# Kernel tuning notes

Hardware: AMD Instinct MI355X
Metric: run time of the kernel (lower is better)

The kernel has to match this reference:

```python
import jax, jax.numpy as jnp
import numpy as np
from jax import lax

DN = ('NCDHW', 'OIDHW', 'NCDHW')
BN_EPS = 1e-5
COS_EPS = 1e-8   # torch CosineSimilarity eps
L1_EPS = 1e-12   # F.normalize default eps


def _lrelu(x):
    return jnp.where(x >= 0, x, 0.2 * x)


def _bn(x, g, b):
    # BatchNorm3d in training mode: batch statistics over (N, D, H, W)
    m = jnp.mean(x, axis=(0, 2, 3, 4), keepdims=True)
    v = jnp.var(x, axis=(0, 2, 3, 4), keepdims=True)
    return g[None, :, None, None, None] * (x - m) * lax.rsqrt(v + BN_EPS) + b[None, :, None, None, None]


def _conv(x, w, b, stride):
    y = lax.conv_general_dilated(x, w, window_strides=stride, padding=[(1, 1)] * 3,
                                 dimension_numbers=DN)
    return y + b[None, :, None, None, None]


def _convT(x, w, b, stride, out_pad):
    # ConvTranspose3d(k=3, padding=1, output_padding=out_pad) == input-dilated conv
    # with flipped kernel and padding (k-1-p, k-1-p+op) = (1, 1+op).
    k = jnp.flip(w, axis=(2, 3, 4))
    y = lax.conv_general_dilated(x, k, window_strides=(1, 1, 1),
                                 padding=[(1, 1 + o) for o in out_pad],
                                 lhs_dilation=stride, dimension_numbers=DN)
    return y + b[None, :, None, None, None]


def setup_inputs() -> dict:
    key = jax.random.key(0)
    ks = jax.random.split(key, 20)
    d = {}
    d['x'] = jax.random.normal(ks[0], (2, 1, 16, 256, 256), jnp.float32)
    enc = [(96, 1), (128, 96), (256, 128), (256, 256)]
    for i, (co, ci) in enumerate(enc):
        fan = ci * 27
        d[f'enc_w{i+1}'] = jax.random.normal(ks[1 + i], (co, ci, 3, 3, 3), jnp.float32) * np.float32(np.sqrt(2.0 / fan))
        d[f'enc_b{i+1}'] = jnp.zeros((co,), jnp.float32)
        d[f'enc_g{i+1}'] = jnp.ones((co,), jnp.float32)
        d[f'enc_be{i+1}'] = jnp.zeros((co,), jnp.float32)
    d['mem'] = jax.random.normal(ks[5], (2000, 256), jnp.float32) * np.float32(1.0 / np.sqrt(256))
    dec = [(256, 256), (128, 256), (96, 128), (1, 96)]  # (Cout, Cin)
    for i, (co, ci) in enumerate(dec):
        fan = ci * 27
        d[f'dec_w{i+1}'] = jax.random.normal(ks[6 + i], (co, ci, 3, 3, 3), jnp.float32) * np.float32(np.sqrt(2.0 / fan))
        d[f'dec_b{i+1}'] = jnp.zeros((co,), jnp.float32)
        if i < 3:
            d[f'dec_g{i+1}'] = jnp.ones((co,), jnp.float32)
            d[f'dec_be{i+1}'] = jnp.zeros((co,), jnp.float32)
    return d


def _forward(x,
             enc_w1, enc_b1, enc_g1, enc_be1,
             enc_w2, enc_b2, enc_g2, enc_be2,
             enc_w3, enc_b3, enc_g3, enc_be3,
             enc_w4, enc_b4, enc_g4, enc_be4,
             mem,
             dec_w1, dec_b1, dec_g1, dec_be1,
             dec_w2, dec_b2, dec_g2, dec_be2,
             dec_w3, dec_b3, dec_g3, dec_be3,
             dec_w4, dec_b4):
    # ---- encoder ----
    f = _lrelu(_bn(_conv(x, enc_w1, enc_b1, (1, 2, 2)), enc_g1, enc_be1))
    f = _lrelu(_bn(_conv(f, enc_w2, enc_b2, (2, 2, 2)), enc_g2, enc_be2))
    f = _lrelu(_bn(_conv(f, enc_w3, enc_b3, (2, 2, 2)), enc_g3, enc_be3))
    f = _lrelu(_bn(_conv(f, enc_w4, enc_b4, (2, 2, 2)), enc_g4, enc_be4))
    # ---- memory addressing (cosine similarity without materializing repeats) ----
    N, C, D, H, W = f.shape
    z = f.transpose(0, 2, 3, 4, 1).reshape(-1, C)                    # [M, C]
    z_norm = jnp.linalg.norm(z, axis=1, keepdims=True)               # [M, 1]
    m_norm = jnp.linalg.norm(mem, axis=1, keepdims=True)             # [K, 1]
    num = z @ mem.T                                                  # [M, K]
    den = jnp.maximum(z_norm * m_norm.T, COS_EPS)
    w = jax.nn.softmax(num / den, axis=1)
    w_hat = jax.nn.relu(w)
    w_hat = w_hat / jnp.maximum(jnp.sum(jnp.abs(w_hat), axis=1, keepdims=True), L1_EPS)
    z_hat = w_hat @ mem                                              # [M, C]
    zf = z_hat.reshape(N, D, H, W, C).transpose(0, 4, 1, 2, 3)
    # ---- decoder ----
    y = _lrelu(_bn(_convT(zf, dec_w1, dec_b1, (2, 2, 2), (1, 1, 1)), dec_g1, dec_be1))
    y = _lrelu(_bn(_convT(y, dec_w2, dec_b2, (2, 2, 2), (1, 1, 1)), dec_g2, dec_be2))
    y = _lrelu(_bn(_convT(y, dec_w3, dec_b3, (2, 2, 2), (1, 1, 1)), dec_g3, dec_be3))
    out = _convT(y, dec_w4, dec_b4, (1, 2, 2), (0, 1, 1))
    return out, w_hat


def reference(x,
              enc_w1, enc_b1, enc_g1, enc_be1,
              enc_w2, enc_b2, enc_g2, enc_be2,
              enc_w3, enc_b3, enc_g3, enc_be3,
              enc_w4, enc_b4, enc_g4, enc_be4,
              mem,
              dec_w1, dec_b1, dec_g1, dec_be1,
              dec_w2, dec_b2, dec_g2, dec_be2,
              dec_w3, dec_b3, dec_g3, dec_be3,
              dec_w4, dec_b4):
    return _forward(x,
                    enc_w1, enc_b1, enc_g1, enc_be1,
                    enc_w2, enc_b2, enc_g2, enc_be2,
                    enc_w3, enc_b3, enc_g3, enc_be3,
                    enc_w4, enc_b4, enc_g4, enc_be4,
                    mem,
                    dec_w1, dec_b1, dec_g1, dec_be1,
                    dec_w2, dec_b2, dec_g2, dec_be2,
                    dec_w3, dec_b3, dec_g3, dec_be3,
                    dec_w4, dec_b4)
```

## Files before the change

kernel.cpp:

```cpp
#include <hip/hip_runtime.h>
#include <math.h>

typedef unsigned short u16;
typedef __bf16 bf16;
typedef bf16 bf16x8 __attribute__((ext_vector_type(8)));
typedef float f32x4 __attribute__((ext_vector_type(4)));
typedef u16 u16x8 __attribute__((ext_vector_type(8)));

__device__ inline float b2f(u16 u){ unsigned x = ((unsigned)u) << 16; return __builtin_bit_cast(float, x); }
__device__ inline u16 f2b(float f){ bf16 b = (bf16)f; return __builtin_bit_cast(u16, b); }
__device__ inline f32x4 mfma16(bf16x8 a, bf16x8 b, f32x4 c){
    return __builtin_amdgcn_mfma_f32_16x16x32_bf16(a, b, c, 0, 0, 0);
}
__device__ inline void unp8(uint4 v, float* f){
    f[0]=__builtin_bit_cast(float, v.x<<16); f[1]=__builtin_bit_cast(float, v.x&0xffff0000u);
    f[2]=__builtin_bit_cast(float, v.y<<16); f[3]=__builtin_bit_cast(float, v.y&0xffff0000u);
    f[4]=__builtin_bit_cast(float, v.z<<16); f[5]=__builtin_bit_cast(float, v.z&0xffff0000u);
    f[6]=__builtin_bit_cast(float, v.w<<16); f[7]=__builtin_bit_cast(float, v.w&0xffff0000u);
}

struct Rep7 {
    const float* src[7];
    u16* dst[7];
    int co[7];
    int ci[7];
};
__global__ __launch_bounds__(256) void repack7_k(Rep7 a)
{
    int w = blockIdx.y;
    const float* src = a.src[w]; u16* dst = a.dst[w];
    int Co = a.co[w], Ci = a.ci[w];
    int tot = 27 * Co * Ci;
    for (int e = blockIdx.x * 256 + threadIdx.x; e < tot; e += gridDim.x * 256) {
        int ci = e % Ci; int t2 = e / Ci; int co = t2 % Co; int tp = t2 / Co;
        dst[e] = f2b(src[(size_t)(co * Ci + ci) * 27 + tp]);
    }
}

template<bool ISCONV, int CK, int BN>
__global__ __launch_bounds__(512) void conv_mfma3_k(
    const u16* __restrict__ in, const u16* __restrict__ wt,
    const float* __restrict__ bias, u16* __restrict__ out,
    float* __restrict__ pm, float* __restrict__ pv,
    int Ci, int Co, int Di, int Hi, int Wi,
    int ld, int lh, int lw, int Do, int Ho, int Wo)
{
    constexpr int NK = CK / 32;
    constexpr int NF = BN / 32;
    __shared__ u16 As[128][CK + 8];
    __shared__ u16 Bs[BN][CK + 8];
    const int tid = threadIdx.x;
    const int mtile = blockIdx.x, co0 = blockIdx.y * BN;
    int pd = 0, ph = 0, pw = 0;
    if (!ISCONV) { int bz = blockIdx.z; pd = bz >> 2; ph = (bz >> 1) & 1; pw = bz & 1; }

    const int arow = tid >> 2, seg = tid & 3;
    int xo, yo, zo, n;
    { int m = mtile * 128 + arow;
      xo = m & ((1 << lw) - 1); m >>= lw;
      yo = m & ((1 << lh) - 1); m >>= lh;
      zo = m & ((1 << ld) - 1); n = m >> ld; }
    const bool isb = arow < BN;

    const int wave = tid >> 6, lane = tid & 63;
    const int wm = wave >> 1, wn = wave & 1;
    const int fr = lane & 15, fs = lane >> 4;

    f32x4 acc[2][NF];
    #pragma unroll
    for (int mf = 0; mf < 2; ++mf)
        #pragma unroll
        for (int nf = 0; nf < NF; ++nf) acc[mf][nf] = f32x4{0,0,0,0};

    const int ntd = ISCONV ? 3 : pd + 1;
    const int nth = ISCONV ? 3 : ph + 1;
    const int ntw = ISCONV ? 3 : pw + 1;
    const int nck = Ci / CK;
    const int T = ntd * nth * ntw * nck;
    const size_t HiWi = (size_t)Hi * Wi;

    int pjd = 0, pjh = 0, pjw = 0, pck = 0;
    uint4 av[NK], bv[NK];

    auto load_panel = [&]() {
        int zi = ISCONV ? 2 * zo + pjd - 1 : zo + (pd ? pjd : 0);
        int wd = ISCONV ? pjd : (pd ? (pjd ? 0 : 2) : 1);
        int yi = ISCONV ? 2 * yo + pjh - 1 : yo + (ph ? pjh : 0);
        int wh = ISCONV ? pjh : (ph ? (pjh ? 0 : 2) : 1);
        int xi = ISCONV ? 2 * xo + pjw - 1 : xo + (pw ? pjw : 0);
        int ww = ISCONV ? pjw : (pw ? (pjw ? 0 : 2) : 1);
        bool va = ((unsigned)zi < (unsigned)Di) && ((unsigned)yi < (unsigned)Hi) &&
                  ((unsigned)xi < (unsigned)Wi);
        size_t abase = 0;
        if (va) abase = (((size_t)(n * Di + zi)) * HiWi + (size_t)yi * Wi + xi) * Ci
                      + (size_t)pck * CK;
        int widx = wd * 9 + wh * 3 + ww;
        size_t bbase = ((size_t)widx * Co + (co0 + arow)) * (size_t)Ci + (size_t)pck * CK;
        #pragma unroll
        for (int k = 0; k < NK; ++k) {
            int col = k * 32 + seg * 8;
            av[k] = va  ? *reinterpret_cast<const uint4*>(in + abase + col) : uint4{0,0,0,0};
            bv[k] = isb ? *reinterpret_cast<const uint4*>(wt + bbase + col) : uint4{0,0,0,0};
        }
        ++pck;
        if (pck == nck) { pck = 0; ++pjw;
            if (pjw == ntw) { pjw = 0; ++pjh;
                if (pjh == nth) { pjh = 0; ++pjd; } } }
    };

    load_panel();
    for (int it = 0; it < T; ++it) {
        __syncthreads();
        #pragma unroll
        for (int k = 0; k < NK; ++k) {
            *reinterpret_cast<uint4*>(&As[arow][k * 32 + seg * 8]) = av[k];
            if (isb) *reinterpret_cast<uint4*>(&Bs[arow][k * 32 + seg * 8]) = bv[k];
        }
        __syncthreads();
        if (it + 1 < T) load_panel();
        #pragma unroll
        for (int k = 0; k < NK; ++k) {
            bf16x8 a0 = *reinterpret_cast<const bf16x8*>(&As[wm * 32      + fr][k * 32 + fs * 8]);
            bf16x8 a1 = *reinterpret_cast<const bf16x8*>(&As[wm * 32 + 16 + fr][k * 32 + fs * 8]);
            #pragma unroll
            for (int nf = 0; nf < NF; ++nf) {
                bf16x8 b = *reinterpret_cast<const bf16x8*>(
                    &Bs[wn * (BN / 2) + nf * 16 + fr][k * 32 + fs * 8]);
                acc[0][nf] = mfma16(a0, b, acc[0][nf]);
                acc[1][nf] = mfma16(a1, b, acc[1][nf]);
            }
        }
    }

    float bi[NF], s[NF], q[NF];
    #pragma unroll
    for (int nf = 0; nf < NF; ++nf) {
        bi[nf] = bias[co0 + wn * (BN / 2) + nf * 16 + fr];
        s[nf] = 0.f; q[nf] = 0.f;
    }
    #pragma unroll
    for (int mf = 0; mf < 2; ++mf) {
        #pragma unroll
        for (int j = 0; j < 4; ++j) {
            int rm = mtile * 128 + wm * 32 + mf * 16 + fs * 4 + j;
            size_t vox;
            if (ISCONV) vox = (size_t)rm;
            else {
                int X = rm & ((1 << lw) - 1); int m2 = rm >> lw;
                int Y = m2 & ((1 << lh) - 1); m2 >>= lh;
                int Z = m2 & ((1 << ld) - 1); int nn = m2 >> ld;
                vox = (((size_t)(nn * Do + (2 * Z + pd))) * Ho + (2 * Y + ph)) * Wo + (2 * X + pw);
            }
            #pragma unroll
            for (int nf = 0; nf < NF; ++nf) {
                float f = acc[mf][nf][j] + bi[nf];
                out[vox * Co + (co0 + wn * (BN / 2) + nf * 16 + fr)] = f2b(f);
                s[nf] += f; q[nf] += f * f;
            }
        }
    }
    __syncthreads();
    float* bnS = reinterpret_cast<float*>(&As[0][0]);
    float* bnQ = bnS + BN * 16;
    #pragma unroll
    for (int nf = 0; nf < NF; ++nf) {
        int cl = wn * (BN / 2) + nf * 16 + fr;
        bnS[cl * 16 + wm * 4 + fs] = s[nf];
        bnQ[cl * 16 + wm * 4 + fs] = q[nf];
    }
    __syncthreads();
    if (tid < BN) {
        float S = 0.f, Q = 0.f;
        #pragma unroll
        for (int i = 0; i < 16; ++i) { S += bnS[tid * 16 + i]; Q += bnQ[tid * 16 + i]; }
        int p = blockIdx.x + gridDim.x * (blockIdx.y + gridDim.y * blockIdx.z);
        pm[(size_t)p * BN + tid] = S;
        pv[(size_t)p * BN + tid] = Q;
    }
}

__global__ __launch_bounds__(256) void enc1_k(
    const float* __restrict__ x, const float* __restrict__ w,
    const float* __restrict__ bias, u16* __restrict__ out)
{
    __shared__ uint4 smem[256 * 13];
    float* Xi = reinterpret_cast<float*>(smem);
    const int tid = threadIdx.x;
    int t = blockIdx.x;
    const int tx = t & 7; t >>= 3;
    const int ty = t & 15; t >>= 4;
    const int tz = t;
    const int n = blockIdx.y;
    const int z0 = tz * 2, y0 = ty * 8, x0 = tx * 16;
    for (int i = tid; i < 2244; i += 256) {
        int fz = i / 561; int r = i - fz * 561; int fy = r / 33; int fx = r - fy * 33;
        int zi = z0 - 1 + fz, yi = 2 * y0 - 1 + fy, xi = 2 * x0 - 1 + fx;
        float v = 0.f;
        if ((unsigned)zi < 16u && (unsigned)yi < 256u && (unsigned)xi < 256u)
            v = x[((size_t)(n * 16 + zi) * 256 + yi) * 256 + xi];
        Xi[i] = v;
    }
    __syncthreads();
    const int lx = tid & 15, ly = (tid >> 4) & 7, lz = tid >> 7;
    float iv[27];
    #pragma unroll
    for (int kd = 0; kd < 3; ++kd)
        #pragma unroll
        for (int kh = 0; kh < 3; ++kh)
            #pragma unroll
            for (int kw = 0; kw < 3; ++kw)
                iv[kd * 9 + kh * 3 + kw] = Xi[(lz + kd) * 561 + (2 * ly + kh) * 33 + (2 * lx + kw)];
    __syncthreads();
    #pragma unroll
    for (int og = 0; og < 12; ++og) {
        u16x8 pk;
        #pragma unroll
        for (int oo = 0; oo < 8; ++oo) {
            int o = og * 8 + oo;
            float a = bias[o];
            #pragma unroll
            for (int tp = 0; tp < 27; ++tp) a += iv[tp] * w[o * 27 + tp];
            pk[oo] = f2b(a);
        }
        smem[tid * 13 + og] = __builtin_bit_cast(uint4, pk);
    }
    __syncthreads();
    #pragma unroll
    for (int it = 0; it < 12; ++it) {
        int i = it * 256 + tid;
        int r = i / 192, j = i - r * 192;
        int rz = r >> 3, ry = r & 7;
        int v = r * 16 + j / 12, c8 = j % 12;
        uint4 val = smem[v * 13 + c8];
        size_t voxbase = ((size_t)(n * 16 + z0 + rz) * 128 + (y0 + ry)) * 128 + x0;
        *reinterpret_cast<uint4*>(out + voxbase * 96 + (size_t)j * 8) = val;
    }
}

__global__ __launch_bounds__(256) void dec4g_k(
    const u16* __restrict__ in, const u16* __restrict__ wt4,
    const float* __restrict__ sc, const float* __restrict__ sb,
    float* __restrict__ P)
{
    __shared__ u16 As[64][120];
    __shared__ u16 Bs[32][120];
    const int tid = threadIdx.x;
    const int vox0 = blockIdx.x << 6;
    for (int i = tid; i < 384; i += 256) {
        int row = i / 12, seg = i - row * 12;
        uint4 v = {0,0,0,0};
        if (row < 27) v = *reinterpret_cast<const uint4*>(wt4 + row * 96 + seg * 8);
        *reinterpret_cast<uint4*>(&Bs[row][seg * 8]) = v;
    }
    for (int i = tid; i < 768; i += 256) {
        int row = i / 12, seg = i - row * 12;
        uint4 v = *reinterpret_cast<const uint4*>(in + (size_t)(vox0 + row) * 96 + seg * 8);
        float f[8]; unp8(v, f);
        int c0 = seg * 8;
        u16x8 pk;
        #pragma unroll
        for (int e = 0; e < 8; ++e) {
            float y = f[e] * sc[c0 + e] + sb[c0 + e];
            y = y >= 0.f ? y : 0.2f * y;
            pk[e] = f2b(y);
        }
        *reinterpret_cast<u16x8*>(&As[row][seg * 8]) = pk;
    }
    __syncthreads();
    const int wave = tid >> 6, lane = tid & 63;
    const int fr = lane & 15, fs = lane >> 4;
    f32x4 acc0 = {0,0,0,0}, acc1 = {0,0,0,0};
    #pragma unroll
    for (int kk = 0; kk < 3; ++kk) {
        bf16x8 a  = *reinterpret_cast<const bf16x8*>(&As[wave * 16 + fr][kk * 32 + fs * 8]);
        bf16x8 b0 = *reinterpret_cast<const bf16x8*>(&Bs[fr     ][kk * 32 + fs * 8]);
        bf16x8 b1 = *reinterpret_cast<const bf16x8*>(&Bs[16 + fr][kk * 32 + fs * 8]);
        acc0 = mfma16(a, b0, acc0);
        acc1 = mfma16(a, b1, acc1);
    }
    #pragma unroll
    for (int j = 0; j < 4; ++j) {
        int vox = vox0 + wave * 16 + fs * 4 + j;
        P[(size_t)vox * 32 + fr]      = acc0[j];
        P[(size_t)vox * 32 + 16 + fr] = acc1[j];
    }
}

__global__ __launch_bounds__(256) void dec4s_k(
    const float* __restrict__ P, const float* __restrict__ bias,
    float* __restrict__ out)
{
    __shared__ float Pl[180 * 33];
    const int tid = threadIdx.x;
    int b = blockIdx.x;
    const int tx = b & 15; b >>= 4;
    const int ty = b & 31; b >>= 5;
    const int tz = b;
    const int n = blockIdx.y;
    const int Z0 = tz * 2, Y0 = ty * 8, X0 = tx * 16;
    const int yi0 = Y0 >> 1, xi0 = X0 >> 1;
    for (int i = tid; i < 5760; i += 256) {
        int row = i >> 5, c = i & 31;
        int dz = row / 45; int r = row - dz * 45; int dy = r / 9; int dx = r - dy * 9;
        int zi = Z0 - 1 + dz, yi = yi0 + dy, xi = xi0 + dx;
        float v = 0.f;
        if (zi >= 0 && zi < 16 && yi < 128 && xi < 128)
            v = P[((size_t)((n * 16 + zi) * 128 + yi) * 128 + xi) * 32 + c];
        Pl[row * 33 + c] = v;
    }
    __syncthreads();
    const int lx = tid & 15, ly = (tid >> 4) & 7, lz = tid >> 7;
    float acc = bias[0];
    #pragma unroll
    for (int qd = 0; qd < 3; ++qd) {
        int t = Z0 + lz + qd - 1;
        if (t < 0 || t >= 16) continue;
        int dz = lz + qd;
        #pragma unroll
        for (int qh = 0; qh < 3; ++qh) {
            int u = ly + qh - 1;
            if (u & 1) continue;
            int dy = u >> 1;
            #pragma unroll
            for (int qw = 0; qw < 3; ++qw) {
                int v = lx + qw - 1;
                if (v & 1) continue;
                int dx = v >> 1;
                int widx = (2 - qd) * 9 + (2 - qh) * 3 + (2 - qw);
                acc += Pl[(dz * 45 + dy * 9 + dx) * 33 + widx];
            }
        }
    }
    out[((size_t)(n * 16 + Z0 + lz) * 256 + (Y0 + ly)) * 256 + (X0 + lx)] = acc;
}

__global__ __launch_bounds__(256) void bnstat_k(
    const u16* __restrict__ a, float* __restrict__ pm, float* __restrict__ pv,
    int C, unsigned total8)
{
    __shared__ float sS[256][8];
    __shared__ float sQ[256][8];
    unsigned g = blockIdx.x * 256 + threadIdx.x;
    unsigned stride = gridDim.x * 256;
    float s[8] = {0,0,0,0,0,0,0,0}, q[8] = {0,0,0,0,0,0,0,0};
    for (unsigned i = g; i < total8; i += stride) {
        uint4 v = *reinterpret_cast<const uint4*>(a + (size_t)i * 8);
        float f[8]; unp8(v, f);
        #pragma unroll
        for (int e = 0; e < 8; ++e) { s[e] += f[e]; q[e] += f[e] * f[e]; }
    }
    #pragma unroll
    for (int e = 0; e < 8; ++e) { sS[threadIdx.x][e] = s[e]; sQ[threadIdx.x][e] = q[e]; }
    __syncthreads();
    int c = threadIdx.x;
    if (c < C) {
        int C8 = C >> 3;
        int B = (int)((blockIdx.x * 2048u) % (unsigned)C);
        int r = c - B; r %= C; if (r < 0) r += C;
        int e = r & 7, t0 = r >> 3;
        float S = 0.f, Q = 0.f;
        for (int tt = t0; tt < 256; tt += C8) { S += sS[tt][e]; Q += sQ[tt][e]; }
        pm[blockIdx.x * C + c] = S;
        pv[blockIdx.x * C + c] = Q;
    }
}

__global__ __launch_bounds__(64) void bnfin_k(
    const float* __restrict__ pm, const float* __restrict__ pv,
    const float* __restrict__ g, const float* __restrict__ be,
    float* __restrict__ sc, float* __restrict__ sb, int C, int G, float invcnt)
{
    int c = blockIdx.x;
    float S = 0.f, Q = 0.f;
    for (int b = threadIdx.x; b < G; b += 64) { S += pm[b * C + c]; Q += pv[b * C + c]; }
    #pragma unroll
    for (int off = 32; off; off >>= 1) {
        S += __shfl_down(S, off, 64);
        Q += __shfl_down(Q, off, 64);
    }
    if (threadIdx.x == 0) {
        float m = S * invcnt;
        float v = Q * invcnt - m * m;
        float s = g[c] * rsqrtf(v + 1e-5f);
        sc[c] = s; sb[c] = be[c] - m * s;
    }
}

__global__ __launch_bounds__(64) void bnfin3_k(
    const float* __restrict__ pm, const float* __restrict__ pv,
    const float* __restrict__ g, const float* __restrict__ be,
    float* __restrict__ sc, float* __restrict__ sb,
    int C, int BNl, int gx, int gy, int gz, float invcnt)
{
    int c = blockIdx.x;
    int cog = c / BNl, cl = c % BNl;
    int tot = gx * gz;
    float S = 0.f, Q = 0.f;
    for (int i = threadIdx.x; i < tot; i += 64) {
        int bx = i % gx, bz = i / gx;
        int p = bx + gx * (cog + gy * bz);
        S += pm[(size_t)p * BNl + cl];
        Q += pv[(size_t)p * BNl + cl];
    }
    #pragma unroll
    for (int off = 32; off; off >>= 1) {
        S += __shfl_down(S, off, 64);
        Q += __shfl_down(Q, off, 64);
    }
    if (threadIdx.x == 0) {
        float m = S * invcnt;
        float v = Q * invcnt - m * m;
        float s = g[c] * rsqrtf(v + 1e-5f);
        sc[c] = s; sb[c] = be[c] - m * s;
    }
}

__global__ __launch_bounds__(256) void bnapply_k(
    u16* __restrict__ a, const float* __restrict__ sc, const float* __restrict__ sb,
    int C, unsigned total8)
{
    unsigned g = blockIdx.x * 256 + threadIdx.x;
    unsigned stride = gridDim.x * 256;
    int c0 = (int)((g * 8u) % (unsigned)C);
    float lsc[8], lsb[8];
    #pragma unroll
    for (int e = 0; e < 8; ++e) { lsc[e] = sc[c0 + e]; lsb[e] = sb[c0 + e]; }
    for (unsigned i = g; i < total8; i += stride) {
        uint4 v = *reinterpret_cast<const uint4*>(a + (size_t)i * 8);
        float f[8]; unp8(v, f);
        u16x8 pk;
        #pragma unroll
        for (int e = 0; e < 8; ++e) {
            float y = f[e] * lsc[e] + lsb[e];
            y = y >= 0.f ? y : 0.2f * y;
            pk[e] = f2b(y);
        }
        *reinterpret_cast<u16x8*>(a + (size_t)i * 8) = pk;
    }
}

__global__ __launch_bounds__(256) void memprep_k(
    const float* __restrict__ mem, u16* __restrict__ memb, u16* __restrict__ memT,
    float* __restrict__ mnorm)
{
    int k = blockIdx.x, c = threadIdx.x;
    if (k >= 2000) { memT[(size_t)c * 2048 + k] = 0; return; }
    float v = mem[(size_t)k * 256 + c];
    u16 b = f2b(v);
    memb[(size_t)k * 256 + c] = b;
    memT[(size_t)c * 2048 + k] = b;
    float s = v * v;
    #pragma unroll
    for (int off = 32; off; off >>= 1) s += __shfl_down(s, off, 64);
    __shared__ float red[4];
    if ((c & 63) == 0) red[c >> 6] = s;
    __syncthreads();
    if (c == 0) mnorm[k] = sqrtf(red[0] + red[1] + red[2] + red[3]);
}

__global__ __launch_bounds__(64) void znorm_k(
    const u16* __restrict__ z, float* __restrict__ znorm)
{
    int m = blockIdx.x, l = threadIdx.x;
    ushort4 v = *reinterpret_cast<const ushort4*>(z + (size_t)m * 256 + l * 4);
    float a = b2f(v.x), b = b2f(v.y), cc = b2f(v.z), d = b2f(v.w);
    float s = a * a + b * b + cc * cc + d * d;
    #pragma unroll
    for (int off = 32; off; off >>= 1) s += __shfl_down(s, off, 64);
    if (l == 0) znorm[m] = sqrtf(s);
}

__global__ __launch_bounds__(256) void scores_mfma_k(
    const u16* __restrict__ z, const u16* __restrict__ memb,
    const float* __restrict__ znorm, const float* __restrict__ mnorm,
    float* __restrict__ scores)
{
    __shared__ u16 As[64][40];
    __shared__ u16 Bs[64][40];
    const int tid = threadIdx.x;
    const int m0 = blockIdx.x << 6, n0 = blockIdx.y << 6;
    const int arow = tid >> 2, seg = tid & 3;
    const bool bok = (n0 + arow) < 2000;
    const int wave = tid >> 6, lane = tid & 63;
    const int wm = wave >> 1, wn = wave & 1, fr = lane & 15, fs = lane >> 4;
    f32x4 acc00 = {0,0,0,0}, acc01 = {0,0,0,0}, acc10 = {0,0,0,0}, acc11 = {0,0,0,0};
    for (int k0 = 0; k0 < 256; k0 += 32) {
        uint4 avv = *reinterpret_cast<const uint4*>(z + (size_t)(m0 + arow) * 256 + k0 + seg * 8);
        uint4 bvv = {0,0,0,0};
        if (bok) bvv = *reinterpret_cast<const uint4*>(memb + (size_t)(n0 + arow) * 256 + k0 + seg * 8);
        __syncthreads();
        *reinterpret_cast<uint4*>(&As[arow][seg * 8]) = avv;
        *reinterpret_cast<uint4*>(&Bs[arow][seg * 8]) = bvv;
        __syncthreads();
        bf16x8 a0 = *reinterpret_cast<const bf16x8*>(&As[wm * 32      + fr][fs * 8]);
        bf16x8 a1 = *reinterpret_cast<const bf16x8*>(&As[wm * 32 + 16 + fr][fs * 8]);
        bf16x8 b0 = *reinterpret_cast<const bf16x8*>(&Bs[wn * 32      + fr][fs * 8]);
        bf16x8 b1 = *reinterpret_cast<const bf16x8*>(&Bs[wn * 32 + 16 + fr][fs * 8]);
        acc00 = mfma16(a0, b0, acc00);
        acc01 = mfma16(a0, b1, acc01);
        acc10 = mfma16(a1, b0, acc10);
        acc11 = mfma16(a1, b1, acc11);
    }
    const int c0 = n0 + wn * 32 + fr, c1 = c0 + 16;
    float mn0 = (c0 < 2000) ? mnorm[c0] : 1.f;
    float mn1 = (c1 < 2000) ? mnorm[c1] : 1.f;
    #pragma unroll
    for (int mi = 0; mi < 2; ++mi) {
        f32x4 aN0 = mi ? acc10 : acc00;
        f32x4 aN1 = mi ? acc11 : acc01;
        #pragma unroll
        for (int j = 0; j < 4; ++j) {
            int rm = m0 + wm * 32 + mi * 16 + fs * 4 + j;
            float zn = znorm[rm];
            if (c0 < 2000) scores[(size_t)rm * 2000 + c0] = aN0[j] / fmaxf(zn * mn0, 1e-8f);
            if (c1 < 2000) scores[(size_t)rm * 2000 + c1] = aN1[j] / fmaxf(zn * mn1, 1e-8f);
        }
    }
}

__global__ __launch_bounds__(256) void softmax2_k(
    float* __restrict__ w, u16* __restrict__ wb16)
{
    __shared__ float red[4];
    const int m = blockIdx.x, t = threadIdx.x;
    const bool act = t < 250;
    float v[8];
    if (act) {
        float4 p0 = *reinterpret_cast<const float4*>(w + (size_t)m * 2000 + t * 8);
        float4 p1 = *reinterpret_cast<const float4*>(w + (size_t)m * 2000 + t * 8 + 4);
        v[0]=p0.x; v[1]=p0.y; v[2]=p0.z; v[3]=p0.w;
        v[4]=p1.x; v[5]=p1.y; v[6]=p1.z; v[7]=p1.w;
    } else {
        for (int i = 0; i < 8; ++i) v[i] = -1e30f;
    }
    float mx = -1e30f;
    for (int i = 0; i < 8; ++i) mx = fmaxf(mx, v[i]);
    #pragma unroll
    for (int off = 32; off; off >>= 1) mx = fmaxf(mx, __shfl_down(mx, off, 64));
    if ((t & 63) == 0) red[t >> 6] = mx;
    __syncthreads();
    mx = fmaxf(fmaxf(red[0], red[1]), fmaxf(red[2], red[3]));
    __syncthreads();
    float e[8], sm = 0.f;
    for (int i = 0; i < 8; ++i) {
        e[i] = act ? expf(v[i] - mx) : 0.f;
        sm += e[i];
    }
    #pragma unroll
    for (int off = 32; off; off >>= 1) sm += __shfl_down(sm, off, 64);
    if ((t & 63) == 0) red[t >> 6] = sm;
    __syncthreads();
    float inv = 1.0f / (red[0] + red[1] + red[2] + red[3]);
    u16x8 pk = {0,0,0,0,0,0,0,0};
    if (act) {
        float r[8];
        for (int i = 0; i < 8; ++i) { r[i] = e[i] * inv; pk[i] = f2b(r[i]); }
        float4 o0, o1;
        o0.x=r[0]; o0.y=r[1]; o0.z=r[2]; o0.w=r[3];
        o1.x=r[4]; o1.y=r[5]; o1.z=r[6]; o1.w=r[7];
        *reinterpret_cast<float4*>(w + (size_t)m * 2000 + t * 8)     = o0;
        *reinterpret_cast<float4*>(w + (size_t)m * 2000 + t * 8 + 4) = o1;
    }
    *reinterpret_cast<u16x8*>(wb16 + (size_t)m * 2048 + t * 8) = pk;
}

__global__ __launch_bounds__(256) void zhat_mfma_k(
    const u16* __restrict__ wb16, const u16* __restrict__ memT,
    u16* __restrict__ zf)
{
    __shared__ u16 As[64][40];
    __shared__ u16 Bs[64][40];
    const int tid = threadIdx.x;
    const int m0 = blockIdx.x << 6, n0 = blockIdx.y << 6;
    const int arow = tid >> 2, seg = tid & 3;
    const int wave = tid >> 6, lane = tid & 63;
    const int wm = wave >> 1, wn = wave & 1, fr = lane & 15, fs = lane >> 4;
    f32x4 acc00 = {0,0,0,0}, acc01 = {0,0,0,0}, acc10 = {0,0,0,0}, acc11 = {0,0,0,0};
    for (int k0 = 0; k0 < 2048; k0 += 32) {
        uint4 avv = *reinterpret_cast<const uint4*>(wb16 + (size_t)(m0 + arow) * 2048 + k0 + seg * 8);
        uint4 bvv = *reinterpret_cast<const uint4*>(memT + (size_t)(n0 + arow) * 2048 + k0 + seg * 8);
        __syncthreads();
        *reinterpret_cast<uint4*>(&As[arow][seg * 8]) = avv;
        *reinterpret_cast<uint4*>(&Bs[arow][seg * 8]) = bvv;
        __syncthreads();
        bf16x8 a0 = *reinterpret_cast<const bf16x8*>(&As[wm * 32      + fr][fs * 8]);
        bf16x8 a1 = *reinterpret_cast<const bf16x8*>(&As[wm * 32 + 16 + fr][fs * 8]);
        bf16x8 b0 = *reinterpret_cast<const bf16x8*>(&Bs[wn * 32      + fr][fs * 8]);
        bf16x8 b1 = *reinterpret_cast<const bf16x8*>(&Bs[wn * 32 + 16 + fr][fs * 8]);
        acc00 = mfma16(a0, b0, acc00);
        acc01 = mfma16(a0, b1, acc01);
        acc10 = mfma16(a1, b0, acc10);
        acc11 = mfma16(a1, b1, acc11);
    }
    const int c0 = n0 + wn * 32 + fr, c1 = c0 + 16;
    #pragma unroll
    for (int mi = 0; mi < 2; ++mi) {
        f32x4 aN0 = mi ? acc10 : acc00;
        f32x4 aN1 = mi ? acc11 : acc01;
        #pragma unroll
        for (int j = 0; j < 4; ++j) {
            int rm = m0 + wm * 32 + mi * 16 + fs * 4 + j;
            zf[(size_t)rm * 256 + c0] = f2b(aN0[j]);
            zf[(size_t)rm * 256 + c1] = f2b(aN1[j]);
        }
    }
}

extern "C" void kernel_launch(void* const* d_in, const int* in_sizes, int n_in,
                              void* d_out, int out_size, void* d_ws, size_t ws_size,
                              hipStream_t stream)
{
    const float* x     = (const float*)d_in[0];
    const float* ew[4] = { (const float*)d_in[1],  (const float*)d_in[5],
                           (const float*)d_in[9],  (const float*)d_in[13] };
    const float* eb[4] = { (const float*)d_in[2],  (const float*)d_in[6],
                           (const float*)d_in[10], (const float*)d_in[14] };
    const float* eg[4] = { (const float*)d_in[3],  (const float*)d_in[7],
                           (const float*)d_in[11], (const float*)d_in[15] };
    const float* ebe[4]= { (const float*)d_in[4],  (const float*)d_in[8],
                           (const float*)d_in[12], (const float*)d_in[16] };
    const float* mem   = (const float*)d_in[17];
    const float* dw[4] = { (const float*)d_in[18], (const float*)d_in[22],
                           (const float*)d_in[26], (const float*)d_in[30] };
    const float* db[4] = { (const float*)d_in[19], (const float*)d_in[23],
                           (const float*)d_in[27], (const float*)d_in[31] };
    const float* dg[3] = { (const float*)d_in[20], (const float*)d_in[24],
                           (const float*)d_in[28] };
    const float* dbe[3]= { (const float*)d_in[21], (const float*)d_in[25],
                           (const float*)d_in[29] };

    float* outp  = (float*)d_out;
    float* w_out = (float*)d_out + 2097152;

    char* p = (char*)d_ws;
    auto take = [&](size_t bytes) -> char* {
        char* q = p; p += (bytes + 255) & ~(size_t)255; return q;
    };
    u16* b1   = (u16*)take(50331648ull * 2);
    u16* b2   = (u16*)take(8388608ull * 2);
    u16* b3   = (u16*)take(2097152ull * 2);
    u16* b4   = (u16*)take(262144ull * 2);
    u16* zf   = (u16*)take(262144ull * 2);
    u16* w2   = (u16*)take(331776ull * 2);
    u16* w3   = (u16*)take(884736ull * 2);
    u16* w4   = (u16*)take(1769472ull * 2);
    u16* wd1  = (u16*)take(1769472ull * 2);
    u16* wd2  = (u16*)take(884736ull * 2);
    u16* wd3  = (u16*)take(331776ull * 2);
    u16* wd4  = (u16*)take(2592ull * 2);
    u16* memb = (u16*)take(512000ull * 2);
    u16* memT = (u16*)take(524288ull * 2);
    u16* wb16 = (u16*)take(2097152ull * 2);
    float* P     = (float*)take(16777216ull * 4);
    float* pm    = (float*)take(1048576ull * 4);
    float* pv    = (float*)take(1048576ull * 4);
    float* scb   = (float*)take(7 * 512 * 4);
    float* mnorm = (float*)take(2048 * 4);
    float* znorm = (float*)take(1024 * 4);

    auto SC = [&](int l) { return scb + l * 512; };
    auto SB = [&](int l) { return scb + l * 512 + 256; };

    auto bnc = [&](u16* buf, const float* g, const float* be, int C, int BNl,
                   unsigned total8, int G, int gx, int gy, int gz, int slot, bool apply) {
        bnfin3_k<<<C, 64, 0, stream>>>(pm, pv, g, be, SC(slot), SB(slot),
                                       C, BNl, gx, gy, gz,
                                       (float)C / ((float)total8 * 8.0f));
        if (apply) bnapply_k<<<G, 256, 0, stream>>>(buf, SC(slot), SB(slot), C, total8);
    };

    Rep7 ra;
    ra.src[0]=ew[1]; ra.dst[0]=w2;  ra.co[0]=128; ra.ci[0]=96;
    ra.src[1]=ew[2]; ra.dst[1]=w3;  ra.co[1]=256; ra.ci[1]=128;
    ra.src[2]=ew[3]; ra.dst[2]=w4;  ra.co[2]=256; ra.ci[2]=256;
    ra.src[3]=dw[0]; ra.dst[3]=wd1; ra.co[3]=256; ra.ci[3]=256;
    ra.src[4]=dw[1]; ra.dst[4]=wd2; ra.co[4]=128; ra.ci[4]=256;
    ra.src[5]=dw[2]; ra.dst[5]=wd3; ra.co[5]=96;  ra.ci[5]=128;
    ra.src[6]=dw[3]; ra.dst[6]=wd4; ra.co[6]=1;   ra.ci[6]=96;
    repack7_k<<<dim3(64, 7), 256, 0, stream>>>(ra);
    memprep_k<<<2048, 256, 0, stream>>>(mem, memb, memT, mnorm);

    enc1_k<<<dim3(1024, 2), 256, 0, stream>>>(x, ew[0], eb[0], b1);
    bnstat_k<<<768, 256, 0, stream>>>(b1, pm, pv, 96, 6291456u);
    bnfin_k<<<96, 64, 0, stream>>>(pm, pv, eg[0], ebe[0], SC(0), SB(0), 96, 768,
                                   96.0f / (6291456.0f * 8.0f));
    bnapply_k<<<768, 256, 0, stream>>>(b1, SC(0), SB(0), 96, 6291456u);

    conv_mfma3_k<true, 96, 128><<<dim3(512, 1, 1), 512, 0, stream>>>(
        b1, w2, eb[1], b2, pm, pv, 96, 128, 16, 128, 128, 3, 6, 6, 8, 64, 64);
    bnc(b2, eg[1], ebe[1], 128, 128, 1048576u, 512, 512, 1, 1, 1, true);

    conv_mfma3_k<true, 128, 64><<<dim3(64, 4, 1), 512, 0, stream>>>(
        b2, w3, eb[2], b3, pm, pv, 128, 256, 8, 64, 64, 2, 5, 5, 4, 32, 32);
    bnc(b3, eg[2], ebe[2], 256, 64, 262144u, 512, 64, 4, 1, 2, true);

    conv_mfma3_k<true, 128, 64><<<dim3(8, 4, 1), 512, 0, stream>>>(
        b3, w4, eb[3], b4, pm, pv, 256, 256, 4, 32, 32, 1, 4, 4, 2, 16, 16);
    bnc(b4, eg[3], ebe[3], 256, 64, 32768u, 128, 8, 4, 1, 3, true);

    znorm_k<<<1024, 64, 0, stream>>>(b4, znorm);
    scores_mfma_k<<<dim3(16, 32), 256, 0, stream>>>(b4, memb, znorm, mnorm, w_out);
    softmax2_k<<<1024, 256, 0, stream>>>(w_out, wb16);
    zhat_mfma_k<<<dim3(16, 4), 256, 0, stream>>>(wb16, memT, zf);

    conv_mfma3_k<false, 128, 64><<<dim3(8, 4, 8), 512, 0, stream>>>(
        zf, wd1, db[0], b3, pm, pv, 256, 256, 2, 16, 16, 1, 4, 4, 4, 32, 32);
    bnc(b3, dg[0], dbe[0], 256, 64, 262144u, 512, 8, 4, 8, 4, true);

    conv_mfma3_k<false, 128, 64><<<dim3(64, 2, 8), 512, 0, stream>>>(
        b3, wd2, db[1], b2, pm, pv, 256, 128, 4, 32, 32, 2, 5, 5, 8, 64, 64);
    bnc(b2, dg[1], dbe[1], 128, 64, 1048576u, 512, 64, 2, 8, 5, true);

    conv_mfma3_k<false, 128, 96><<<dim3(512, 1, 8), 512, 0, stream>>>(
        b2, wd3, db[2], b1, pm, pv, 128, 96, 8, 64, 64, 3, 6, 6, 16, 128, 128);
    bnc(b1, dg[2], dbe[2], 96, 96, 6291456u, 768, 512, 1, 8, 6, false);

    dec4g_k<<<8192, 256, 0, stream>>>(b1, wd4, SC(6), SB(6), P);
    dec4s_k<<<dim3(4096, 2), 256, 0, stream>>>(P, db[3], outp);
}
```

Baseline: 693.4 us.

## Fuse enc1 BN statistics into conv kernel and swizzle MFMA block order

Removes the separate bnstat pass over the 96-channel enc1 output. enc1_k now reduces per-block channel sums and sums of squares from the tile it already holds in shared memory and writes 2048 partials, which bnfin then reduces. Separately, the MFMA conv remaps blockIdx.x so that consecutive blocks are spread across the M dimension in 8 groups, presumably to change cache and channel locality. The added reduction runs on only 96 threads looping over 256 voxels, which lengthens the enc1 tail. The remap also assumes gridDim.x is divisible by 8.

```diff
diff --git a/kernel.cpp b/kernel.cpp
--- a/kernel.cpp
+++ b/kernel.cpp
@@ -50,7 +50,10 @@
     __shared__ u16 As[128][CK + 8];
     __shared__ u16 Bs[BN][CK + 8];
     const int tid = threadIdx.x;
-    const int mtile = blockIdx.x, co0 = blockIdx.y * BN;
+    const int gx = gridDim.x;
+    const int bxr = blockIdx.x;
+    const int mtile = (bxr & 7) * (gx >> 3) + (bxr >> 3);
+    const int co0 = blockIdx.y * BN;
     int pd = 0, ph = 0, pw = 0;
     if (!ISCONV) { int bz = blockIdx.z; pd = bz >> 2; ph = (bz >> 1) & 1; pw = bz & 1; }
 
@@ -181,7 +184,8 @@
 
 __global__ __launch_bounds__(256) void enc1_k(
     const float* __restrict__ x, const float* __restrict__ w,
-    const float* __restrict__ bias, u16* __restrict__ out)
+    const float* __restrict__ bias, u16* __restrict__ out,
+    float* __restrict__ pm, float* __restrict__ pv)
 {
     __shared__ uint4 smem[256 * 13];
     float* Xi = reinterpret_cast<float*>(smem);
@@ -234,6 +238,18 @@
         uint4 val = smem[v * 13 + c8];
         size_t voxbase = ((size_t)(n * 16 + z0 + rz) * 128 + (y0 + ry)) * 128 + x0;
         *reinterpret_cast<uint4*>(out + voxbase * 96 + (size_t)j * 8) = val;
+    }
+    if (tid < 96) {
+        int c8 = tid >> 3, ce = tid & 7;
+        float S = 0.f, Q = 0.f;
+        for (int t2 = 0; t2 < 256; ++t2) {
+            u16x8 pk = __builtin_bit_cast(u16x8, smem[t2 * 13 + c8]);
+            float f = b2f(pk[ce]);
+            S += f; Q += f * f;
+        }
+        int blk = blockIdx.x + gridDim.x * blockIdx.y;
+        pm[(size_t)blk * 96 + tid] = S;
+        pv[(size_t)blk * 96 + tid] = Q;
     }
 }
 
@@ -332,37 +348,6 @@
         }
     }
     out[((size_t)(n * 16 + Z0 + lz) * 256 + (Y0 + ly)) * 256 + (X0 + lx)] = acc;
-}
-
-__global__ __launch_bounds__(256) void bnstat_k(
-    const u16* __restrict__ a, float* __restrict__ pm, float* __restrict__ pv,
-    int C, unsigned total8)
-{
-    __shared__ float sS[256][8];
-    __shared__ float sQ[256][8];
-    unsigned g = blockIdx.x * 256 + threadIdx.x;
-    unsigned stride = gridDim.x * 256;
-    float s[8] = {0,0,0,0,0,0,0,0}, q[8] = {0,0,0,0,0,0,0,0};
-    for (unsigned i = g; i < total8; i += stride) {
-        uint4 v = *reinterpret_cast<const uint4*>(a + (size_t)i * 8);
-        float f[8]; unp8(v, f);
-        #pragma unroll
-        for (int e = 0; e < 8; ++e) { s[e] += f[e]; q[e] += f[e] * f[e]; }
-    }
-    #pragma unroll
-    for (int e = 0; e < 8; ++e) { sS[threadIdx.x][e] = s[e]; sQ[threadIdx.x][e] = q[e]; }
-    __syncthreads();
-    int c = threadIdx.x;
-    if (c < C) {
-        int C8 = C >> 3;
-        int B = (int)((blockIdx.x * 2048u) % (unsigned)C);
-        int r = c - B; r %= C; if (r < 0) r += C;
-        int e = r & 7, t0 = r >> 3;
-        float S = 0.f, Q = 0.f;
-        for (int tt = t0; tt < 256; tt += C8) { S += sS[tt][e]; Q += sQ[tt][e]; }
-        pm[blockIdx.x * C + c] = S;
-        pv[blockIdx.x * C + c] = Q;
-    }
 }
 
 __global__ __launch_bounds__(64) void bnfin_k(
@@ -680,9 +665,8 @@
     repack7_k<<<dim3(64, 7), 256, 0, stream>>>(ra);
     memprep_k<<<2048, 256, 0, stream>>>(mem, memb, memT, mnorm);
 
-    enc1_k<<<dim3(1024, 2), 256, 0, stream>>>(x, ew[0], eb[0], b1);
-    bnstat_k<<<768, 256, 0, stream>>>(b1, pm, pv, 96, 6291456u);
-    bnfin_k<<<96, 64, 0, stream>>>(pm, pv, eg[0], ebe[0], SC(0), SB(0), 96, 768,
+    enc1_k<<<dim3(1024, 2), 256, 0, stream>>>(x, ew[0], eb[0], b1, pm, pv);
+    bnfin_k<<<96, 64, 0, stream>>>(pm, pv, eg[0], ebe[0], SC(0), SB(0), 96, 2048,
                                    96.0f / (6291456.0f * 8.0f));
     bnapply_k<<<768, 256, 0, stream>>>(b1, SC(0), SB(0), 96, 6291456u);
 
```

Result: slower. 707.6 us (+2.1%).
